# Kernel tuning notes

Hardware: AMD Instinct MI355X
Metric: run time of the kernel (lower is better)

Reference implementation:

```python
import jax, jax.numpy as jnp
import numpy as np

N_NODES = 10000
N_EDGES = 640000
IN_C = 128
HID = 256
OUT_C = 256


def _linear_params(key, fan_in, fan_out):
    k1, k2 = jax.random.split(key)
    bound = 1.0 / np.sqrt(fan_in)
    W = jax.random.uniform(k1, (fan_in, fan_out), jnp.float32, -bound, bound)
    b = jax.random.uniform(k2, (fan_out,), jnp.float32, -bound, bound)
    return W, b


def setup_inputs() -> dict:
    key = jax.random.key(0)
    ks = jax.random.split(key, 8)
    x = jax.random.normal(ks[0], (N_NODES, IN_C), jnp.float32)
    edge_index = jax.random.randint(ks[1], (2, N_EDGES), 0, N_NODES, jnp.int32)
    W0a, b0a = _linear_params(ks[2], IN_C, HID)
    W0b, b0b = _linear_params(ks[3], HID, HID)
    W1a, b1a = _linear_params(ks[4], HID, HID)
    W1b, b1b = _linear_params(ks[5], HID, HID)
    W2a, b2a = _linear_params(ks[6], HID, OUT_C)
    W2b, b2b = _linear_params(ks[7], OUT_C, OUT_C)
    return {"x": x, "edge_index": edge_index,
            "W0a": W0a, "b0a": b0a, "W0b": W0b, "b0b": b0b,
            "W1a": W1a, "b1a": b1a, "W1b": W1b, "b1b": b1b,
            "W2a": W2a, "b2a": b2a, "W2b": W2b, "b2b": b2b}


def _gin_conv(x, src, dst, Wa, ba, Wb, bb):
    # sum-aggregate neighbor features: agg[i] = sum_{(j->i) in E} x[j]
    agg = jax.ops.segment_sum(x[src], dst, num_segments=N_NODES)
    h = x + agg  # eps = 0 (PyG GINConv default): (1+eps)*x + agg
    h = jnp.maximum(h @ Wa + ba, 0.0) @ Wb + bb  # Linear-ReLU-Linear MLP
    return h


def reference(x, edge_index, W0a, b0a, W0b, b0b, W1a, b1a, W1b, b1b, W2a, b2a, W2b, b2b):
    src, dst = edge_index[0], edge_index[1]
    h = _gin_conv(x, src, dst, W0a, b0a, W0b, b0b)
    h = jnp.maximum(h, 0.0)  # ReLU; dropout is identity in eval mode
    h = _gin_conv(h, src, dst, W1a, b1a, W1b, b1b)
    h = jnp.maximum(h, 0.0)
    h = _gin_conv(h, src, dst, W2a, b2a, W2b, b2b)
    return h
```

## Files before the change

### kernel.cpp

```cpp
#include <hip/hip_runtime.h>

#define N_NODES 10000
#define N_EDGES 640000
#define ELL_W   128
#define NB      157
#define BCAP    4600
#define LCAP    80
#define CHUNK   2500

typedef short short8 __attribute__((ext_vector_type(8)));
typedef float f32x4 __attribute__((ext_vector_type(4)));

__device__ inline float bf2f(unsigned short u) {
    return __uint_as_float(((unsigned)u) << 16);
}
__device__ inline unsigned short f2bf(float f) {
    unsigned u = __float_as_uint(f);
    u += 0x7fffu + ((u >> 16) & 1u);
    return (unsigned short)(u >> 16);
}

__global__ __launch_bounds__(256) void bin_edges(const int* __restrict__ src,
                                                 const int* __restrict__ dst,
                                                 int* __restrict__ gCursor,
                                                 unsigned* __restrict__ gBucket) {
    __shared__ unsigned bins[NB][LCAP];
    __shared__ int cnt[NB];
    __shared__ int base[NB];
    int t = threadIdx.x;
    for (int i = t; i < NB; i += 256) cnt[i] = 0;
    __syncthreads();

    int e0 = blockIdx.x * CHUNK;
    int e1 = min(e0 + CHUNK, N_EDGES);
    for (int e = e0 + t; e < e1; e += 256) {
        int d = dst[e];
        int b = d >> 6;
        unsigned pk = ((unsigned)src[e] << 6) | (unsigned)(d & 63);
        int p = atomicAdd(&cnt[b], 1);
        if (p < LCAP) bins[b][p] = pk;
    }
    __syncthreads();
    for (int i = t; i < NB; i += 256) {
        int c = min(cnt[i], LCAP);
        cnt[i] = c;
        base[i] = atomicAdd(&gCursor[i], c);
    }
    __syncthreads();
    int wave = t >> 6, lane = t & 63;
    for (int b = wave; b < NB; b += 4) {
        int ba = base[b];
        int n = min(cnt[b], max(0, BCAP - ba));
        for (int i = lane; i < n; i += 64)
            gBucket[(size_t)b * BCAP + ba + i] = bins[b][i];
    }
}

__global__ __launch_bounds__(256) void build_ell(const unsigned* __restrict__ gBucket,
                                                 const int* __restrict__ gCursor,
                                                 unsigned short* __restrict__ ell,
                                                 int* __restrict__ deg) {
    __shared__ unsigned short rows[64 * ELL_W];
    __shared__ int ldeg[64];
    int b = blockIdx.x;
    int t = threadIdx.x;
    for (int i = t; i < 64; i += 256) ldeg[i] = 0;
    __syncthreads();

    int n = min(gCursor[b], BCAP);
    const unsigned* bk = gBucket + (size_t)b * BCAP;
    for (int i = t; i < n; i += 256) {
        unsigned pk = bk[i];
        int local = pk & 63;
        int s = pk >> 6;
        int p = atomicAdd(&ldeg[local], 1);
        if (p < ELL_W) rows[local * ELL_W + p] = (unsigned short)s;
    }
    __syncthreads();

    int node0 = b * 64;
    int nNodes = min(64, N_NODES - node0);
    if (nNodes <= 0) return;
    for (int i = t; i < nNodes; i += 256)
        deg[node0 + i] = min(ldeg[i], ELL_W);
    int totalVec = nNodes * (ELL_W / 8);
    short8* dstv = (short8*)(ell + (size_t)node0 * ELL_W);
    const short8* srcv = (const short8*)rows;
    for (int i = t; i < totalVec; i += 256) dstv[i] = srcv[i];
}

struct WList {
    const float* src[6];
    unsigned short* dst[6];
    int K[6];
    int off[7];
};

__global__ __launch_bounds__(256) void prep_kernel(const float4* __restrict__ x,
                                                   ushort4* __restrict__ xb, int n4,
                                                   WList wl, int totalW,
                                                   int* __restrict__ gCursor) {
    int idx = blockIdx.x * 256 + threadIdx.x;
    if (blockIdx.x == 0 && threadIdx.x < NB) gCursor[threadIdx.x] = 0;
    if (idx < n4) {
        float4 v = x[idx];
        ushort4 o;
        o.x = f2bf(v.x); o.y = f2bf(v.y); o.z = f2bf(v.z); o.w = f2bf(v.w);
        xb[idx] = o;
        return;
    }
    int r0 = idx - n4;
    if (r0 >= totalW) return;
    int w = 0;
    while (r0 >= wl.off[w + 1]) ++w;
    int r = r0 - wl.off[w];
    int k = r >> 8;
    int n = r & 255;
    wl.dst[w][(size_t)n * wl.K[w] + k] = f2bf(wl.src[w][r]);
}

template <int U2STRIDE>
__global__ __launch_bounds__(256) void gather_ell(const unsigned* __restrict__ x,
                                                  const unsigned short* __restrict__ ell,
                                                  const int* __restrict__ deg,
                                                  unsigned* __restrict__ out) {
    int wid = (blockIdx.x * 256 + threadIdx.x) >> 6;
    int lane = threadIdx.x & 63;
    if (wid >= N_NODES) return;
    int off = blockIdx.y * 64 + lane;

    unsigned v = x[(size_t)wid * U2STRIDE + off];
    float a0 = bf2f((unsigned short)(v & 0xffff));
    float a1 = bf2f((unsigned short)(v >> 16));

    int dg = min(deg[wid], ELL_W);
    const unsigned short* row = ell + (size_t)wid * ELL_W;

    int j = 0;
    for (; j + 32 <= dg; j += 32) {
        short8 i0 = *(const short8*)(row + j);
        short8 i1 = *(const short8*)(row + j + 8);
        short8 i2 = *(const short8*)(row + j + 16);
        short8 i3 = *(const short8*)(row + j + 24);
        unsigned vv[32];
#pragma unroll
        for (int q = 0; q < 8; ++q)
            vv[q] = x[(size_t)(unsigned short)i0[q] * U2STRIDE + off];
#pragma unroll
        for (int q = 0; q < 8; ++q)
            vv[8 + q] = x[(size_t)(unsigned short)i1[q] * U2STRIDE + off];
#pragma unroll
        for (int q = 0; q < 8; ++q)
            vv[16 + q] = x[(size_t)(unsigned short)i2[q] * U2STRIDE + off];
#pragma unroll
        for (int q = 0; q < 8; ++q)
            vv[24 + q] = x[(size_t)(unsigned short)i3[q] * U2STRIDE + off];
#pragma unroll
        for (int q = 0; q < 32; ++q) {
            a0 += bf2f((unsigned short)(vv[q] & 0xffff));
            a1 += bf2f((unsigned short)(vv[q] >> 16));
        }
    }
    for (; j + 16 <= dg; j += 16) {
        short8 iA = *(const short8*)(row + j);
        short8 iB = *(const short8*)(row + j + 8);
        unsigned vv[16];
#pragma unroll
        for (int q = 0; q < 8; ++q)
            vv[q] = x[(size_t)(unsigned short)iA[q] * U2STRIDE + off];
#pragma unroll
        for (int q = 0; q < 8; ++q)
            vv[8 + q] = x[(size_t)(unsigned short)iB[q] * U2STRIDE + off];
#pragma unroll
        for (int q = 0; q < 16; ++q) {
            a0 += bf2f((unsigned short)(vv[q] & 0xffff));
            a1 += bf2f((unsigned short)(vv[q] >> 16));
        }
    }
    for (; j + 4 <= dg; j += 4) {
        ushort4 sA = *(const ushort4*)(row + j);
        unsigned v0 = x[(size_t)sA.x * U2STRIDE + off];
        unsigned v1 = x[(size_t)sA.y * U2STRIDE + off];
        unsigned v2 = x[(size_t)sA.z * U2STRIDE + off];
        unsigned v3 = x[(size_t)sA.w * U2STRIDE + off];
        a0 += (bf2f((unsigned short)(v0 & 0xffff)) + bf2f((unsigned short)(v1 & 0xffff))) +
              (bf2f((unsigned short)(v2 & 0xffff)) + bf2f((unsigned short)(v3 & 0xffff)));
        a1 += (bf2f((unsigned short)(v0 >> 16)) + bf2f((unsigned short)(v1 >> 16))) +
              (bf2f((unsigned short)(v2 >> 16)) + bf2f((unsigned short)(v3 >> 16)));
    }
    for (; j < dg; ++j) {
        unsigned vv = x[(size_t)row[j] * U2STRIDE + off];
        a0 += bf2f((unsigned short)(vv & 0xffff));
        a1 += bf2f((unsigned short)(vv >> 16));
    }
    unsigned o = (unsigned)f2bf(a0) | ((unsigned)f2bf(a1) << 16);
    out[(size_t)wid * U2STRIDE + off] = o;
}

template <int KSTEPS, bool RELU2, bool F32OUT>
__global__ __launch_bounds__(256) void mlp_mfma(const unsigned short* __restrict__ A,
                                                const unsigned short* __restrict__ WtA,
                                                const float* __restrict__ biasA,
                                                const unsigned short* __restrict__ WtB,
                                                const float* __restrict__ biasB,
                                                void* __restrict__ Cout) {
    constexpr int K1 = KSTEPS * 32;
    constexpr int LP = 264;
    __shared__ unsigned short hid[32 * LP];

    int r0 = blockIdx.x * 32;
    int tid = threadIdx.x;
    int lane = tid & 63;
    int nq = tid >> 6;
    int lrow = lane & 15;
    int lkg = lane >> 4;
    int n0 = nq * 64;

    {
        const short8* Ap0 = (const short8*)(A + (size_t)(r0 + lrow) * K1 + lkg * 8);
        const short8* Ap1 = (const short8*)(A + (size_t)(r0 + 16 + lrow) * K1 + lkg * 8);
        const short8* Bp = (const short8*)(WtA + (size_t)(n0 + lrow) * K1 + lkg * 8);
        f32x4 acc[2][4] = {};
#pragma unroll
        for (int ks = 0; ks < KSTEPS; ++ks) {
            short8 a0 = Ap0[ks * 4];
            short8 a1 = Ap1[ks * 4];
            short8 b0 = Bp[ks * 4 + 0 * 2 * K1];
            short8 b1 = Bp[ks * 4 + 1 * 2 * K1];
            short8 b2 = Bp[ks * 4 + 2 * 2 * K1];
            short8 b3 = Bp[ks * 4 + 3 * 2 * K1];
            acc[0][0] = __builtin_amdgcn_mfma_f32_16x16x32_bf16(a0, b0, acc[0][0], 0, 0, 0);
            acc[0][1] = __builtin_amdgcn_mfma_f32_16x16x32_bf16(a0, b1, acc[0][1], 0, 0, 0);
            acc[0][2] = __builtin_amdgcn_mfma_f32_16x16x32_bf16(a0, b2, acc[0][2], 0, 0, 0);
            acc[0][3] = __builtin_amdgcn_mfma_f32_16x16x32_bf16(a0, b3, acc[0][3], 0, 0, 0);
            acc[1][0] = __builtin_amdgcn_mfma_f32_16x16x32_bf16(a1, b0, acc[1][0], 0, 0, 0);
            acc[1][1] = __builtin_amdgcn_mfma_f32_16x16x32_bf16(a1, b1, acc[1][1], 0, 0, 0);
            acc[1][2] = __builtin_amdgcn_mfma_f32_16x16x32_bf16(a1, b2, acc[1][2], 0, 0, 0);
            acc[1][3] = __builtin_amdgcn_mfma_f32_16x16x32_bf16(a1, b3, acc[1][3], 0, 0, 0);
        }
#pragma unroll
        for (int rg = 0; rg < 2; ++rg) {
            int row = rg * 16 + lkg * 4;
#pragma unroll
            for (int nt = 0; nt < 4; ++nt) {
                int c = n0 + nt * 16 + lrow;
                float bv = biasA[c];
#pragma unroll
                for (int r = 0; r < 4; ++r) {
                    float v = fmaxf(acc[rg][nt][r] + bv, 0.f);
                    hid[(row + r) * LP + c] = f2bf(v);
                }
            }
        }
    }
    __syncthreads();

    {
        const short8* Bp = (const short8*)(WtB + (size_t)(n0 + lrow) * 256 + lkg * 8);
        f32x4 acc[2][4] = {};
#pragma unroll
        for (int ks = 0; ks < 8; ++ks) {
            short8 a0 = *(const short8*)&hid[lrow * LP + ks * 32 + lkg * 8];
            short8 a1 = *(const short8*)&hid[(16 + lrow) * LP + ks * 32 + lkg * 8];
            short8 b0 = Bp[ks * 4 + 0 * 2 * 256];
            short8 b1 = Bp[ks * 4 + 1 * 2 * 256];
            short8 b2 = Bp[ks * 4 + 2 * 2 * 256];
            short8 b3 = Bp[ks * 4 + 3 * 2 * 256];
            acc[0][0] = __builtin_amdgcn_mfma_f32_16x16x32_bf16(a0, b0, acc[0][0], 0, 0, 0);
            acc[0][1] = __builtin_amdgcn_mfma_f32_16x16x32_bf16(a0, b1, acc[0][1], 0, 0, 0);
            acc[0][2] = __builtin_amdgcn_mfma_f32_16x16x32_bf16(a0, b2, acc[0][2], 0, 0, 0);
            acc[0][3] = __builtin_amdgcn_mfma_f32_16x16x32_bf16(a0, b3, acc[0][3], 0, 0, 0);
            acc[1][0] = __builtin_amdgcn_mfma_f32_16x16x32_bf16(a1, b0, acc[1][0], 0, 0, 0);
            acc[1][1] = __builtin_amdgcn_mfma_f32_16x16x32_bf16(a1, b1, acc[1][1], 0, 0, 0);
            acc[1][2] = __builtin_amdgcn_mfma_f32_16x16x32_bf16(a1, b2, acc[1][2], 0, 0, 0);
            acc[1][3] = __builtin_amdgcn_mfma_f32_16x16x32_bf16(a1, b3, acc[1][3], 0, 0, 0);
        }
#pragma unroll
        for (int rg = 0; rg < 2; ++rg) {
            int orow = r0 + rg * 16 + lkg * 4;
#pragma unroll
            for (int nt = 0; nt < 4; ++nt) {
                int c = n0 + nt * 16 + lrow;
                float bv = biasB[c];
#pragma unroll
                for (int r = 0; r < 4; ++r) {
                    int grow = orow + r;
                    if (grow >= N_NODES) continue;
                    float v = acc[rg][nt][r] + bv;
                    if (RELU2) v = fmaxf(v, 0.f);
                    if (F32OUT)
                        ((float*)Cout)[(size_t)grow * 256 + c] = v;
                    else
                        ((unsigned short*)Cout)[(size_t)grow * 256 + c] = f2bf(v);
                }
            }
        }
    }
}

extern "C" void kernel_launch(void* const* d_in, const int* in_sizes, int n_in,
                              void* d_out, int out_size, void* d_ws, size_t ws_size,
                              hipStream_t stream) {
    const float* x   = (const float*)d_in[0];
    const int*   ei  = (const int*)d_in[1];
    const int*   src = ei;
    const int*   dst = ei + N_EDGES;
    const float* W0a = (const float*)d_in[2];
    const float* b0a = (const float*)d_in[3];
    const float* W0b = (const float*)d_in[4];
    const float* b0b = (const float*)d_in[5];
    const float* W1a = (const float*)d_in[6];
    const float* b1a = (const float*)d_in[7];
    const float* W1b = (const float*)d_in[8];
    const float* b1b = (const float*)d_in[9];
    const float* W2a = (const float*)d_in[10];
    const float* b2a = (const float*)d_in[11];
    const float* W2b = (const float*)d_in[12];
    const float* b2b = (const float*)d_in[13];

    char* ws = (char*)d_ws;
    size_t off = 0;
    auto alloc = [&](size_t bytes) {
        void* p = ws + off;
        off += (bytes + 255) & ~(size_t)255;
        return p;
    };
    unsigned short* xb    = (unsigned short*)alloc((size_t)N_NODES * 128 * 2);
    unsigned short* B0    = (unsigned short*)alloc((size_t)N_NODES * 256 * 2);
    unsigned short* B2    = (unsigned short*)alloc((size_t)N_NODES * 256 * 2);
    unsigned short* Wt0a  = (unsigned short*)alloc(256 * 128 * 2);
    unsigned short* Wt0b  = (unsigned short*)alloc(256 * 256 * 2);
    unsigned short* Wt1a  = (unsigned short*)alloc(256 * 256 * 2);
    unsigned short* Wt1b  = (unsigned short*)alloc(256 * 256 * 2);
    unsigned short* Wt2a  = (unsigned short*)alloc(256 * 256 * 2);
    unsigned short* Wt2b  = (unsigned short*)alloc(256 * 256 * 2);
    int*            deg   = (int*)alloc(N_NODES * 4);
    unsigned short* ell   = (unsigned short*)alloc((size_t)N_NODES * ELL_W * 2);
    int*            gCur  = (int*)alloc(NB * 4);
    unsigned*       gBkt  = (unsigned*)alloc((size_t)NB * BCAP * 4);

    dim3 gatherGrid1((N_NODES + 3) / 4, 1);
    dim3 gatherGrid2((N_NODES + 3) / 4, 2);
    int mlpBlocks = (N_NODES + 31) / 32;

    WList wl;
    wl.src[0] = W0a; wl.dst[0] = Wt0a; wl.K[0] = 128;
    wl.src[1] = W0b; wl.dst[1] = Wt0b; wl.K[1] = 256;
    wl.src[2] = W1a; wl.dst[2] = Wt1a; wl.K[2] = 256;
    wl.src[3] = W1b; wl.dst[3] = Wt1b; wl.K[3] = 256;
    wl.src[4] = W2a; wl.dst[4] = Wt2a; wl.K[4] = 256;
    wl.src[5] = W2b; wl.dst[5] = Wt2b; wl.K[5] = 256;
    int totalW = 0;
    for (int i = 0; i < 6; ++i) { wl.off[i] = totalW; totalW += wl.K[i] * 256; }
    wl.off[6] = totalW;
    int n4 = N_NODES * 128 / 4;
    int prepTasks = n4 + totalW;
    prep_kernel<<<(prepTasks + 255) / 256, 256, 0, stream>>>(
        (const float4*)x, (ushort4*)xb, n4, wl, totalW, gCur);

    bin_edges<<<(N_EDGES + CHUNK - 1) / CHUNK, 256, 0, stream>>>(src, dst, gCur, gBkt);
    build_ell<<<NB, 256, 0, stream>>>(gBkt, gCur, ell, deg);

    gather_ell<64><<<gatherGrid1, 256, 0, stream>>>((const unsigned*)xb, ell, deg, (unsigned*)B0);
    mlp_mfma<4, true, false><<<mlpBlocks, 256, 0, stream>>>(B0, Wt0a, b0a, Wt0b, b0b, B2);
    gather_ell<128><<<gatherGrid2, 256, 0, stream>>>((const unsigned*)B2, ell, deg, (unsigned*)B0);
    mlp_mfma<8, true, false><<<mlpBlocks, 256, 0, stream>>>(B0, Wt1a, b1a, Wt1b, b1b, B2);
    gather_ell<128><<<gatherGrid2, 256, 0, stream>>>((const unsigned*)B2, ell, deg, (unsigned*)B0);
    mlp_mfma<8, false, true><<<mlpBlocks, 256, 0, stream>>>(B0, Wt2a, b2a, Wt2b, b2b, d_out);
}
```

Before: 161.0 us.

## Build ELL adjacency with a single global-atomic scatter kernel

Replaces the two-pass graph build (bin edges into per-64-node buckets in shared memory, then build ELL rows per bucket) with one kernel. That kernel does a global atomicAdd on each destination's degree counter and writes the source index straight into the ELL row. Degree counters are now zeroed in the prep kernel. This removes one launch and the intermediate bucket buffer traffic, at the cost of global atomic contention and scattered 2-byte writes. Degrees are also no longer clamped to the ELL width, and neighbor order becomes nondeterministic.

```diff
diff --git a/kernel.cpp b/kernel.cpp
--- a/kernel.cpp
+++ b/kernel.cpp
@@ -3,10 +3,6 @@
 #define N_NODES 10000
 #define N_EDGES 640000
 #define ELL_W   128
-#define NB      157
-#define BCAP    4600
-#define LCAP    80
-#define CHUNK   2500
 
 typedef short short8 __attribute__((ext_vector_type(8)));
 typedef float f32x4 __attribute__((ext_vector_type(4)));
@@ -20,73 +16,15 @@
     return (unsigned short)(u >> 16);
 }
 
-__global__ __launch_bounds__(256) void bin_edges(const int* __restrict__ src,
-                                                 const int* __restrict__ dst,
-                                                 int* __restrict__ gCursor,
-                                                 unsigned* __restrict__ gBucket) {
-    __shared__ unsigned bins[NB][LCAP];
-    __shared__ int cnt[NB];
-    __shared__ int base[NB];
-    int t = threadIdx.x;
-    for (int i = t; i < NB; i += 256) cnt[i] = 0;
-    __syncthreads();
-
-    int e0 = blockIdx.x * CHUNK;
-    int e1 = min(e0 + CHUNK, N_EDGES);
-    for (int e = e0 + t; e < e1; e += 256) {
-        int d = dst[e];
-        int b = d >> 6;
-        unsigned pk = ((unsigned)src[e] << 6) | (unsigned)(d & 63);
-        int p = atomicAdd(&cnt[b], 1);
-        if (p < LCAP) bins[b][p] = pk;
-    }
-    __syncthreads();
-    for (int i = t; i < NB; i += 256) {
-        int c = min(cnt[i], LCAP);
-        cnt[i] = c;
-        base[i] = atomicAdd(&gCursor[i], c);
-    }
-    __syncthreads();
-    int wave = t >> 6, lane = t & 63;
-    for (int b = wave; b < NB; b += 4) {
-        int ba = base[b];
-        int n = min(cnt[b], max(0, BCAP - ba));
-        for (int i = lane; i < n; i += 64)
-            gBucket[(size_t)b * BCAP + ba + i] = bins[b][i];
-    }
-}
-
-__global__ __launch_bounds__(256) void build_ell(const unsigned* __restrict__ gBucket,
-                                                 const int* __restrict__ gCursor,
-                                                 unsigned short* __restrict__ ell,
-                                                 int* __restrict__ deg) {
-    __shared__ unsigned short rows[64 * ELL_W];
-    __shared__ int ldeg[64];
-    int b = blockIdx.x;
-    int t = threadIdx.x;
-    for (int i = t; i < 64; i += 256) ldeg[i] = 0;
-    __syncthreads();
-
-    int n = min(gCursor[b], BCAP);
-    const unsigned* bk = gBucket + (size_t)b * BCAP;
-    for (int i = t; i < n; i += 256) {
-        unsigned pk = bk[i];
-        int local = pk & 63;
-        int s = pk >> 6;
-        int p = atomicAdd(&ldeg[local], 1);
-        if (p < ELL_W) rows[local * ELL_W + p] = (unsigned short)s;
-    }
-    __syncthreads();
-
-    int node0 = b * 64;
-    int nNodes = min(64, N_NODES - node0);
-    if (nNodes <= 0) return;
-    for (int i = t; i < nNodes; i += 256)
-        deg[node0 + i] = min(ldeg[i], ELL_W);
-    int totalVec = nNodes * (ELL_W / 8);
-    short8* dstv = (short8*)(ell + (size_t)node0 * ELL_W);
-    const short8* srcv = (const short8*)rows;
-    for (int i = t; i < totalVec; i += 256) dstv[i] = srcv[i];
+__global__ __launch_bounds__(256) void fill_ell(const int* __restrict__ src,
+                                                const int* __restrict__ dst,
+                                                int* __restrict__ deg,
+                                                unsigned short* __restrict__ ell) {
+    int e = blockIdx.x * 256 + threadIdx.x;
+    if (e >= N_EDGES) return;
+    int d = dst[e];
+    int pos = atomicAdd(&deg[d], 1);
+    if (pos < ELL_W) ell[(size_t)d * ELL_W + pos] = (unsigned short)src[e];
 }
 
 struct WList {
@@ -99,9 +37,9 @@
 __global__ __launch_bounds__(256) void prep_kernel(const float4* __restrict__ x,
                                                    ushort4* __restrict__ xb, int n4,
                                                    WList wl, int totalW,
-                                                   int* __restrict__ gCursor) {
+                                                   int* __restrict__ deg) {
     int idx = blockIdx.x * 256 + threadIdx.x;
-    if (blockIdx.x == 0 && threadIdx.x < NB) gCursor[threadIdx.x] = 0;
+    if (idx < N_NODES) deg[idx] = 0;
     if (idx < n4) {
         float4 v = x[idx];
         ushort4 o;
@@ -336,12 +274,11 @@
     unsigned short* Wt2b  = (unsigned short*)alloc(256 * 256 * 2);
     int*            deg   = (int*)alloc(N_NODES * 4);
     unsigned short* ell   = (unsigned short*)alloc((size_t)N_NODES * ELL_W * 2);
-    int*            gCur  = (int*)alloc(NB * 4);
-    unsigned*       gBkt  = (unsigned*)alloc((size_t)NB * BCAP * 4);
 
     dim3 gatherGrid1((N_NODES + 3) / 4, 1);
     dim3 gatherGrid2((N_NODES + 3) / 4, 2);
     int mlpBlocks = (N_NODES + 31) / 32;
+    int edgeBlocks = (N_EDGES + 255) / 256;
 
     WList wl;
     wl.src[0] = W0a; wl.dst[0] = Wt0a; wl.K[0] = 128;
@@ -356,10 +293,9 @@
     int n4 = N_NODES * 128 / 4;
     int prepTasks = n4 + totalW;
     prep_kernel<<<(prepTasks + 255) / 256, 256, 0, stream>>>(
-        (const float4*)x, (ushort4*)xb, n4, wl, totalW, gCur);
-
-    bin_edges<<<(N_EDGES + CHUNK - 1) / CHUNK, 256, 0, stream>>>(src, dst, gCur, gBkt);
-    build_ell<<<NB, 256, 0, stream>>>(gBkt, gCur, ell, deg);
+        (const float4*)x, (ushort4*)xb, n4, wl, totalW, deg);
+
+    fill_ell<<<edgeBlocks, 256, 0, stream>>>(src, dst, deg, ell);
 
     gather_ell<64><<<gatherGrid1, 256, 0, stream>>>((const unsigned*)xb, ell, deg, (unsigned*)B0);
     mlp_mfma<4, true, false><<<mlpBlocks, 256, 0, stream>>>(B0, Wt0a, b0a, Wt0b, b0b, B2);
```

New measurement: 177.6 us. +10.3%, slower.
